# Performance work log

Measured on AMD Instinct MI355X. Metric: run time of the kernel, lower is better.

The kernel has to match this reference:

```python
import jax, jax.numpy as jnp
import numpy as np

NEG_SLOPE = 0.01  # F.leaky_relu default


def gcn_conv(x, W, b, src, dst):
    """PyG GCNConv: add self-loops, symmetric deg^-1/2 normalization, linear, scatter-add."""
    n = x.shape[0]
    loop = jnp.arange(n)
    s = jnp.concatenate([src, loop])  # source j
    d = jnp.concatenate([dst, loop])  # target i
    deg = jax.ops.segment_sum(jnp.ones_like(d, dtype=x.dtype), d, num_segments=n)
    dis = jnp.where(deg > 0, jax.lax.rsqrt(jnp.maximum(deg, 1e-12)), 0.0)
    norm = dis[s] * dis[d]                       # [E+N]
    h = x @ W                                    # [N, out]
    msg = h[s] * norm[:, None]                   # gather + scale
    out = jax.ops.segment_sum(msg, d, num_segments=n)  # scatter-add to targets
    return out + b


def setup_inputs() -> dict:
    key = jax.random.key(0)
    ks = jax.random.split(key, 8)
    N, E, G = 100000, 800000, 100
    IN, H, OUT = 128, 256, 16
    x = jax.random.normal(ks[0], (N, IN), dtype=jnp.float32)
    edge_index = jax.random.randint(ks[1], (2, E), 0, N, dtype=jnp.int64)
    batch = jnp.repeat(jnp.arange(G, dtype=jnp.int64), N // G)  # sorted graph ids
    def glorot(k, fi, fo):
        lim = np.sqrt(6.0 / (fi + fo))
        return jax.random.uniform(k, (fi, fo), jnp.float32, -lim, lim)
    return {
        "x": x, "edge_index": edge_index, "batch": batch,
        "W1": glorot(ks[2], IN, H), "b1": jnp.zeros((H,), jnp.float32),
        "W2": glorot(ks[3], H, H),  "b2": jnp.zeros((H,), jnp.float32),
        "W3": glorot(ks[4], H, OUT), "b3": jnp.zeros((OUT,), jnp.float32),
    }


def reference(x, edge_index, batch, W1, b1, W2, b2, W3, b3):
    src, dst = edge_index[0], edge_index[1]
    h = gcn_conv(x, W1, b1, src, dst)
    h = jax.nn.leaky_relu(h, NEG_SLOPE)  # dropout p=0.0 -> identity
    h = gcn_conv(h, W2, b2, src, dst)
    h = jax.nn.leaky_relu(h, NEG_SLOPE)
    h = gcn_conv(h, W3, b3, src, dst)
    # get_zero_nodes: first node of each graph in the sorted batch vector
    mask = jnp.concatenate([jnp.array([True]), batch[1:] != batch[:-1]])
    return h[mask, :]  # [n_graphs, out_channels]
```

## Files before the change

### kernel.cpp

```cpp
#include <hip/hip_runtime.h>

#define NEG_SLOPE 0.01f

using short8 = __attribute__((ext_vector_type(8))) short;
using f32x4  = __attribute__((ext_vector_type(4))) float;

__device__ inline float b2f(ushort u) {
    union { unsigned u; float f; } x; x.u = ((unsigned)u) << 16; return x.f;
}
__device__ inline ushort f2b(float f) {
    union { float f; unsigned u; } x; x.f = f;
    unsigned r = x.u + 0x7FFFu + ((x.u >> 16) & 1u);
    return (ushort)(r >> 16);
}
__device__ inline void gload16(const void* g, void* l) {
    __builtin_amdgcn_global_load_lds((__attribute__((address_space(1))) void*)g,
                                     (__attribute__((address_space(3))) void*)l, 16, 0, 0);
}


__global__ void init_kernel(const int* __restrict__ batch, int* __restrict__ cnt,
                            int* __restrict__ flag1, int* __restrict__ flag2,
                            int* __restrict__ rootflag, int* __restrict__ picked,
                            int4* __restrict__ aggslot, int N) {
    int i = blockIdx.x * blockDim.x + threadIdx.x;
    if (i < 1024) aggslot[i] = make_int4(0, 0, 0, 0);
    if (i >= N) return;
    cnt[i] = 0;
    int root = (i == 0) || (batch[i] != batch[i - 1]);
    flag1[i] = root;
    flag2[i] = 0;
    rootflag[i] = root;
    if (root) picked[batch[i]] = i;
}


__global__ void count_f1(const int* __restrict__ src, const int* __restrict__ dst,
                         const int* __restrict__ rootflag, int* __restrict__ cnt,
                         int* __restrict__ flag1, int E) {
    int i = blockIdx.x * blockDim.x + threadIdx.x;
    int e0 = i * 4;
    if (e0 + 3 < E) {
        int4 dq = *(const int4*)(dst + e0);
        int r0 = rootflag[dq.x], r1 = rootflag[dq.y], r2 = rootflag[dq.z], r3 = rootflag[dq.w];
        atomicAdd(&cnt[dq.x], 1);
        atomicAdd(&cnt[dq.y], 1);
        atomicAdd(&cnt[dq.z], 1);
        atomicAdd(&cnt[dq.w], 1);
        if (r0 | r1 | r2 | r3) {
            int4 sq = *(const int4*)(src + e0);
            if (r0) flag1[sq.x] = 1;
            if (r1) flag1[sq.y] = 1;
            if (r2) flag1[sq.z] = 1;
            if (r3) flag1[sq.w] = 1;
        }
    } else if (e0 < E) {
        for (int e = e0; e < E; e++) {
            int d = dst[e];
            atomicAdd(&cnt[d], 1);
            if (rootflag[d]) flag1[src[e]] = 1;
        }
    }
}


__global__ void frontier2v(const int* __restrict__ src, const int* __restrict__ dst,
                           const int* __restrict__ flag1, int* __restrict__ flag2,
                           int E, int N) {
    int i = blockIdx.x * blockDim.x + threadIdx.x;
    int e0 = i * 4;
    if (e0 + 3 < E) {
        int4 dq = *(const int4*)(dst + e0);
        int f0 = flag1[dq.x], f1 = flag1[dq.y], f2 = flag1[dq.z], f3 = flag1[dq.w];
        if (f0 | f1 | f2 | f3) {
            int4 sq = *(const int4*)(src + e0);
            if (f0) flag2[sq.x] = 1;
            if (f1) flag2[sq.y] = 1;
            if (f2) flag2[sq.z] = 1;
            if (f3) flag2[sq.w] = 1;
        }
    } else if (e0 < E) {
        for (int e = e0; e < E; e++) if (flag1[dst[e]]) flag2[src[e]] = 1;
    }
    if (i < N && flag1[i]) flag2[i] = 1;
}


__global__ __launch_bounds__(256) void scan_one(
    const int* __restrict__ cnt, const int* __restrict__ f1, const int* __restrict__ f2,
    int4* __restrict__ aggslot, float* __restrict__ dis,
    int* __restrict__ rowptr, int* __restrict__ cur,
    int* __restrict__ pos1, int* __restrict__ pos2,
    int* __restrict__ list1, int* __restrict__ list2,
    int* __restrict__ counts, int N, int nb,
    const float* __restrict__ W1, ushort* __restrict__ W1t,
    const float* __restrict__ W2, ushort* __restrict__ W2t) {
    __shared__ int l0[256], l1[256], l2[256];
    __shared__ int baseS[3];
    const int b = blockIdx.x, t = threadIdx.x;
    const int base = b * 1024 + t * 4;

    int c[4] = {0,0,0,0}, a1[4] = {0,0,0,0}, a2[4] = {0,0,0,0};
    if (base + 3 < N) {
        int4 q = *(const int4*)(cnt + base); c[0]=q.x; c[1]=q.y; c[2]=q.z; c[3]=q.w;
        int4 u = *(const int4*)(f1 + base);  a1[0]=u.x; a1[1]=u.y; a1[2]=u.z; a1[3]=u.w;
        int4 v = *(const int4*)(f2 + base);  a2[0]=v.x; a2[1]=v.y; a2[2]=v.z; a2[3]=v.w;
    } else {
        for (int i = 0; i < 4; i++) if (base + i < N) {
            c[i] = cnt[base + i]; a1[i] = f1[base + i]; a2[i] = f2[base + i];
        }
    }
#pragma unroll
    for (int i = 0; i < 4; i++)
        if (base + i < N) dis[base + i] = rsqrtf((float)c[i] + 1.0f);

    int m[4];
#pragma unroll
    for (int i = 0; i < 4; i++) m[i] = a2[i] ? c[i] : 0;
    int ts0 = m[0] + m[1] + m[2] + m[3];
    int ts1 = a1[0] + a1[1] + a1[2] + a1[3];
    int ts2 = a2[0] + a2[1] + a2[2] + a2[3];
    l0[t] = ts0; l1[t] = ts1; l2[t] = ts2;
    __syncthreads();
    for (int off = 1; off < 256; off <<= 1) {
        int u0 = (t >= off) ? l0[t - off] : 0;
        int u1 = (t >= off) ? l1[t - off] : 0;
        int u2 = (t >= off) ? l2[t - off] : 0;
        __syncthreads();
        l0[t] += u0; l1[t] += u1; l2[t] += u2;
        __syncthreads();
    }

    if (t == 0) {
        __hip_atomic_store(&aggslot[b].x, l0[255], __ATOMIC_RELAXED, __HIP_MEMORY_SCOPE_AGENT);
        __hip_atomic_store(&aggslot[b].y, l1[255], __ATOMIC_RELAXED, __HIP_MEMORY_SCOPE_AGENT);
        __hip_atomic_store(&aggslot[b].z, l2[255], __ATOMIC_RELAXED, __HIP_MEMORY_SCOPE_AGENT);
        __hip_atomic_store(&aggslot[b].w, 1, __ATOMIC_RELEASE, __HIP_MEMORY_SCOPE_AGENT);
    }

    if (t < 64) {
        int g0 = 0, g1 = 0, g2 = 0;
        for (int w0 = 0; w0 < b; w0 += 64) {
            int idx = w0 + t;
            if (idx < b) {
                while (__hip_atomic_load(&aggslot[idx].w, __ATOMIC_ACQUIRE,
                                         __HIP_MEMORY_SCOPE_AGENT) == 0) {
                    __builtin_amdgcn_s_sleep(1);
                }
                g0 += __hip_atomic_load(&aggslot[idx].x, __ATOMIC_RELAXED, __HIP_MEMORY_SCOPE_AGENT);
                g1 += __hip_atomic_load(&aggslot[idx].y, __ATOMIC_RELAXED, __HIP_MEMORY_SCOPE_AGENT);
                g2 += __hip_atomic_load(&aggslot[idx].z, __ATOMIC_RELAXED, __HIP_MEMORY_SCOPE_AGENT);
            }
        }
#pragma unroll
        for (int s = 1; s < 64; s <<= 1) {
            g0 += __shfl_xor(g0, s, 64);
            g1 += __shfl_xor(g1, s, 64);
            g2 += __shfl_xor(g2, s, 64);
        }
        if (t == 0) { baseS[0] = g0; baseS[1] = g1; baseS[2] = g2; }
    }
    __syncthreads();

    int run0 = baseS[0] + l0[t] - ts0;
    int run1 = baseS[1] + l1[t] - ts1;
    int run2 = baseS[2] + l2[t] - ts2;
#pragma unroll
    for (int i = 0; i < 4; i++) {
        if (base + i < N) {
            rowptr[base + i] = run0;
            cur[base + i] = run0;
            if (a1[i]) { pos1[base + i] = run1; list1[run1] = base + i; }
            if (a2[i]) { pos2[base + i] = run2; list2[run2] = base + i; }
        }
        run0 += m[i]; run1 += a1[i]; run2 += a2[i];
    }
    if (b == nb - 1 && t == 255) {
        counts[0] = baseS[1] + l1[255];
        counts[1] = baseS[2] + l2[255];
        rowptr[N] = baseS[0] + l0[255];
    }

    for (int idx = b * 256 + t; idx < 98304; idx += gridDim.x * 256) {
        if (idx < 32768) {
            int n = idx >> 7, k = idx & 127;
            W1t[idx] = f2b(W1[k * 256 + n]);
        } else {
            int j = idx - 32768;
            int n = j >> 8, k = j & 255;
            W2t[j] = f2b(W2[k * 256 + n]);
        }
    }
}


__global__ void fill_fv(const int* __restrict__ src, const int* __restrict__ dst,
                        const int* __restrict__ flag2, int* __restrict__ cur,
                        int* __restrict__ col, int E) {
    int i = blockIdx.x * blockDim.x + threadIdx.x;
    int e0 = i * 4;
    if (e0 + 3 < E) {
        int4 dq = *(const int4*)(dst + e0);
        int f0 = flag2[dq.x], f1 = flag2[dq.y], f2 = flag2[dq.z], f3 = flag2[dq.w];
        if (f0 | f1 | f2 | f3) {
            int4 sq = *(const int4*)(src + e0);
            if (f0) col[atomicAdd(&cur[dq.x], 1)] = sq.x;
            if (f1) col[atomicAdd(&cur[dq.y], 1)] = sq.y;
            if (f2) col[atomicAdd(&cur[dq.z], 1)] = sq.z;
            if (f3) col[atomicAdd(&cur[dq.w], 1)] = sq.w;
        }
    } else if (e0 < E) {
        for (int e = e0; e < E; e++) {
            int d = dst[e];
            if (flag2[d]) col[atomicAdd(&cur[d], 1)] = src[e];
        }
    }
}


__global__ __launch_bounds__(256) void aggx_c(const float* __restrict__ x,
                                              const float* __restrict__ dis,
                                              const int* __restrict__ rowptr,
                                              const int* __restrict__ col,
                                              const int* __restrict__ list2,
                                              const int* __restrict__ counts,
                                              ushort* __restrict__ aggXc) {
    const int M2 = counts[1];
    int wave = blockIdx.x * 4 + (threadIdx.x >> 6);
    int lane = threadIdx.x & 63;
    int li = lane & 31, sub = lane >> 5;
    int stride = gridDim.x * 8;
    const float* xp = x + li * 4;
    for (int p = wave * 2 + sub; p < M2; p += stride) {
        int node = list2[p];
        float di = dis[node];
        float4 sv = *(const float4*)(xp + (size_t)node * 128);
        float a0 = di * sv.x, a1 = di * sv.y, a2 = di * sv.z, a3 = di * sv.w;
        int e = rowptr[node], e1 = rowptr[node + 1];
        for (; e + 2 <= e1; e += 2) {
            int s0 = col[e], s1 = col[e + 1];
            float w0 = dis[s0], w1 = dis[s1];
            float4 v0 = *(const float4*)(xp + (size_t)s0 * 128);
            float4 v1 = *(const float4*)(xp + (size_t)s1 * 128);
            a0 += w0 * v0.x + w1 * v1.x;
            a1 += w0 * v0.y + w1 * v1.y;
            a2 += w0 * v0.z + w1 * v1.z;
            a3 += w0 * v0.w + w1 * v1.w;
        }
        if (e < e1) {
            int s = col[e];
            float w = dis[s];
            float4 v = *(const float4*)(xp + (size_t)s * 128);
            a0 += w * v.x; a1 += w * v.y; a2 += w * v.z; a3 += w * v.w;
        }
        ushort4 o;
        o.x = f2b(di * a0); o.y = f2b(di * a1); o.z = f2b(di * a2); o.w = f2b(di * a3);
        *(ushort4*)(aggXc + (size_t)p * 128 + li * 4) = o;
    }
}


__global__ __launch_bounds__(256) void agg2_c(const ushort* __restrict__ h1c,
                                              const float* __restrict__ dis,
                                              const int* __restrict__ rowptr,
                                              const int* __restrict__ col,
                                              const int* __restrict__ list1,
                                              const int* __restrict__ pos2,
                                              const int* __restrict__ counts,
                                              ushort* __restrict__ agg1c) {
    const int M1 = counts[0];
    int wave = blockIdx.x * 4 + (threadIdx.x >> 6);
    int lane = threadIdx.x & 63;
    int li = lane & 31, sub = lane >> 5;
    int stride = gridDim.x * 8;
    const ushort* hp = h1c + (size_t)li * 8;
    for (int p = wave * 2 + sub; p < M1; p += stride) {
        int i = list1[p];
        float di = dis[i];
        float a[8];
        {
            short8 v = *(const short8*)(hp + (size_t)pos2[i] * 256);
#pragma unroll
            for (int j = 0; j < 8; j++) a[j] = b2f((ushort)v[j]);
        }
        int e1 = rowptr[i + 1];
        for (int e = rowptr[i]; e < e1; e++) {
            short8 v = *(const short8*)(hp + (size_t)pos2[col[e]] * 256);
#pragma unroll
            for (int j = 0; j < 8; j++) a[j] += b2f((ushort)v[j]);
        }
        short8 o;
#pragma unroll
        for (int j = 0; j < 8; j++) o[j] = (short)f2b(di * a[j]);
        *(short8*)(agg1c + (size_t)p * 256 + li * 8) = o;
    }
}


template <int K>
__global__ __launch_bounds__(512) void gemm_c(const ushort* __restrict__ A,
                                              const ushort* __restrict__ Bt,
                                              const float* __restrict__ bias,
                                              const float* __restrict__ dis,
                                              const int* __restrict__ list,
                                              const int* __restrict__ counts, int which,
                                              ushort* __restrict__ C) {
    __shared__ ushort As[128 * 64];
    __shared__ ushort Bs[256 * 64];
    const int M = counts[which];
    const int t = threadIdx.x;
    const int lane = t & 63;
    const int w = t >> 6;
    const int wm = w >> 2, wn = w & 3;

    for (int tile = blockIdx.x; tile * 128 < M; tile += gridDim.x) {
        const int row0 = tile * 128;
        f32x4 acc[4][4] = {};

        for (int kt = 0; kt < K / 64; kt++) {
#pragma unroll
            for (int it = 0; it < 2; it++) {
                int q = it * 512 + t;
                int r = q >> 3, c = q & 7;
                int cs = c ^ (r & 7);
                int ga = min(row0 + r, M - 1);
                gload16(A + (size_t)ga * K + kt * 64 + cs * 8, &As[q * 8]);
            }
#pragma unroll
            for (int it = 0; it < 4; it++) {
                int q = it * 512 + t;
                int r = q >> 3, c = q & 7;
                int cs = c ^ (r & 7);
                gload16(Bt + (size_t)r * K + kt * 64 + cs * 8, &Bs[q * 8]);
            }
            __syncthreads();
#pragma unroll
            for (int ks = 0; ks < 2; ks++) {
                short8 a[4], b[4];
                int cc = ks * 4 + (lane >> 4);
#pragma unroll
                for (int m = 0; m < 4; m++) {
                    int R = wm * 64 + m * 16 + (lane & 15);
                    a[m] = *(const short8*)&As[R * 64 + ((cc ^ (R & 7)) * 8)];
                }
#pragma unroll
                for (int n = 0; n < 4; n++) {
                    int R = wn * 64 + n * 16 + (lane & 15);
                    b[n] = *(const short8*)&Bs[R * 64 + ((cc ^ (R & 7)) * 8)];
                }
#pragma unroll
                for (int m = 0; m < 4; m++)
#pragma unroll
                    for (int n = 0; n < 4; n++)
                        acc[m][n] = __builtin_amdgcn_mfma_f32_16x16x32_bf16(a[m], b[n], acc[m][n], 0, 0, 0);
            }
            __syncthreads();
        }

#pragma unroll
        for (int m = 0; m < 4; m++) {
#pragma unroll
            for (int j = 0; j < 4; j++) {
                int grow = row0 + wm * 64 + m * 16 + (lane >> 4) * 4 + j;
                if (grow >= M) continue;
                float dr = dis[list[grow]];
#pragma unroll
                for (int n = 0; n < 4; n++) {
                    int gcol = wn * 64 + n * 16 + (lane & 15);
                    float v = acc[m][n][j] + bias[gcol];
                    v = v > 0.f ? v : NEG_SLOPE * v;
                    C[(size_t)grow * 256 + gcol] = f2b(v * dr);
                }
            }
        }
    }
}


__global__ __launch_bounds__(256) void final_c(const ushort* __restrict__ h2c,
                                               const float* __restrict__ dis,
                                               const int* __restrict__ rowptr,
                                               const int* __restrict__ col,
                                               const int* __restrict__ picked,
                                               const int* __restrict__ pos1,
                                               const float* __restrict__ W3,
                                               const float* __restrict__ b3,
                                               float* __restrict__ out, int G) {
    __shared__ float agg[256];
    __shared__ float red[256];
    int g = blockIdx.x;
    int t = threadIdx.x;
    if (g >= G) return;
    int i = picked[g];
    float di = dis[i];
    float a = b2f(h2c[(size_t)pos1[i] * 256 + t]);
    int e1 = rowptr[i + 1];
    for (int e = rowptr[i]; e < e1; e++) {
        a += b2f(h2c[(size_t)pos1[col[e]] * 256 + t]);
    }
    agg[t] = di * a;
    __syncthreads();
    int c = t & 15, seg = t >> 4;
    float p = 0.f;
#pragma unroll
    for (int kk = 0; kk < 16; kk++) {
        int k = seg * 16 + kk;
        p += agg[k] * W3[k * 16 + c];
    }
    red[t] = p;
    __syncthreads();
    if (t < 16) {
        float sres = 0.f;
#pragma unroll
        for (int ss = 0; ss < 16; ss++) sres += red[ss * 16 + t];
        out[g * 16 + t] = sres + b3[t];
    }
}


extern "C" void kernel_launch(void* const* d_in, const int* in_sizes, int n_in,
                              void* d_out, int out_size, void* d_ws, size_t ws_size,
                              hipStream_t stream) {
    const float* x   = (const float*)d_in[0];
    const int* ei    = (const int*)d_in[1];
    const int* batch = (const int*)d_in[2];
    const float* W1  = (const float*)d_in[3];
    const float* b1  = (const float*)d_in[4];
    const float* W2  = (const float*)d_in[5];
    const float* b2  = (const float*)d_in[6];
    const float* W3  = (const float*)d_in[7];
    const float* b3  = (const float*)d_in[8];

    const int IN = 128, H = 256, OUT = 16;
    int N = in_sizes[0] / IN;
    int E = in_sizes[1] / 2;
    int G = out_size / OUT;
    const int* srcp = ei;
    const int* dstp = ei + E;

    char* p = (char*)d_ws;
    auto carve = [&](size_t bytes) {
        char* q = p;
        p += (bytes + 255) & ~(size_t)255;
        return q;
    };
    int*    cnt      = (int*)carve((size_t)N * 4);
    int*    flag1    = (int*)carve((size_t)N * 4);
    int*    flag2    = (int*)carve((size_t)N * 4);
    int*    rootflag = (int*)carve((size_t)N * 4);
    float*  dis    = (float*)carve((size_t)N * 4);
    int*    rowptr = (int*)carve(((size_t)N + 1) * 4);
    int*    cur    = (int*)carve((size_t)N * 4);
    int4*   aggslot= (int4*)carve(1024 * 16);
    int*    counts = (int*)carve(256);
    int*    picked = (int*)carve((size_t)G * 4);
    int*    pos1   = (int*)carve((size_t)N * 4);
    int*    pos2   = (int*)carve((size_t)N * 4);
    int*    list1  = (int*)carve((size_t)N * 4);
    int*    list2  = (int*)carve((size_t)N * 4);
    int*    col    = (int*)carve((size_t)E * 4);
    ushort* W1t    = (ushort*)carve((size_t)256 * 128 * 2);
    ushort* W2t    = (ushort*)carve((size_t)256 * 256 * 2);
    ushort* RA     = (ushort*)carve((size_t)N * H * 2);
    ushort* RB     = (ushort*)carve((size_t)N * H * 2);

    ushort* aggXc = RA;
    ushort* agg1c = RA;
    ushort* h1c   = RB;
    ushort* h2c   = RB;

    int nb = (N + 1023) / 1024;
    int e4 = (E + 3) / 4;
    int epN = (e4 > N ? e4 : N);

    init_kernel<<<(N + 255) / 256, 256, 0, stream>>>(batch, cnt, flag1, flag2, rootflag,
                                                     picked, aggslot, N);
    count_f1<<<(e4 + 255) / 256, 256, 0, stream>>>(srcp, dstp, rootflag, cnt, flag1, E);
    frontier2v<<<(epN + 255) / 256, 256, 0, stream>>>(srcp, dstp, flag1, flag2, E, N);
    scan_one<<<nb, 256, 0, stream>>>(cnt, flag1, flag2, aggslot, dis, rowptr, cur,
                                     pos1, pos2, list1, list2, counts, N, nb,
                                     W1, W1t, W2, W2t);
    fill_fv<<<(e4 + 255) / 256, 256, 0, stream>>>(srcp, dstp, flag2, cur, col, E);
    aggx_c<<<1024, 256, 0, stream>>>(x, dis, rowptr, col, list2, counts, aggXc);
    gemm_c<128><<<128, 512, 0, stream>>>(aggXc, W1t, b1, dis, list2, counts, 1, h1c);
    agg2_c<<<128, 256, 0, stream>>>(h1c, dis, rowptr, col, list1, pos2, counts, agg1c);
    gemm_c<256><<<64, 512, 0, stream>>>(agg1c, W2t, b2, dis, list1, counts, 0, h2c);
    final_c<<<G, 256, 0, stream>>>(h2c, dis, rowptr, col, picked, pos1, W3, b3, (float*)d_out, G);
}
```

Measured before the change: 131.3 us.

## Fuse tail GEMM/aggregation stages into persistent kernel with grid barriers

Replaces the four tail launches (GEMM1, second aggregation, GEMM2, final readout) with one persistent 64-block kernel that separates phases with atomic grid barriers. It also drops the init kernel in favour of a memset and computes root flags inline from the batch vector. The aim is to cut launch overhead and inter-kernel gaps on a small problem. In exchange, GEMM1 and the aggregation now run on 64 blocks instead of 128, and the spin barriers assume all blocks are co-resident.

```diff
diff --git a/kernel.cpp b/kernel.cpp
--- a/kernel.cpp
+++ b/kernel.cpp
@@ -17,32 +17,34 @@
     __builtin_amdgcn_global_load_lds((__attribute__((address_space(1))) void*)g,
                                      (__attribute__((address_space(3))) void*)l, 16, 0, 0);
 }
-
-
-__global__ void init_kernel(const int* __restrict__ batch, int* __restrict__ cnt,
-                            int* __restrict__ flag1, int* __restrict__ flag2,
-                            int* __restrict__ rootflag, int* __restrict__ picked,
-                            int4* __restrict__ aggslot, int N) {
+__device__ inline int isroot(const int* __restrict__ batch, int d) {
+    return (d == 0) || (batch[d] != batch[d - 1]);
+}
+__device__ inline void gbar(int* ctr, int nblk) {
+    __syncthreads();
+    if (threadIdx.x == 0) {
+        __threadfence();
+        __hip_atomic_fetch_add(ctr, 1, __ATOMIC_RELEASE, __HIP_MEMORY_SCOPE_AGENT);
+        while (__hip_atomic_load(ctr, __ATOMIC_ACQUIRE, __HIP_MEMORY_SCOPE_AGENT) < nblk)
+            __builtin_amdgcn_s_sleep(1);
+    }
+    __syncthreads();
+}
+
+
+__global__ void count_f1(const int* __restrict__ src, const int* __restrict__ dst,
+                         const int* __restrict__ batch, int* __restrict__ cnt,
+                         int* __restrict__ flag1, int* __restrict__ picked, int E, int N) {
     int i = blockIdx.x * blockDim.x + threadIdx.x;
-    if (i < 1024) aggslot[i] = make_int4(0, 0, 0, 0);
-    if (i >= N) return;
-    cnt[i] = 0;
-    int root = (i == 0) || (batch[i] != batch[i - 1]);
-    flag1[i] = root;
-    flag2[i] = 0;
-    rootflag[i] = root;
-    if (root) picked[batch[i]] = i;
-}
-
-
-__global__ void count_f1(const int* __restrict__ src, const int* __restrict__ dst,
-                         const int* __restrict__ rootflag, int* __restrict__ cnt,
-                         int* __restrict__ flag1, int E) {
-    int i = blockIdx.x * blockDim.x + threadIdx.x;
+    if (i < N && isroot(batch, i)) {
+        picked[batch[i]] = i;
+        flag1[i] = 1;
+    }
     int e0 = i * 4;
     if (e0 + 3 < E) {
         int4 dq = *(const int4*)(dst + e0);
-        int r0 = rootflag[dq.x], r1 = rootflag[dq.y], r2 = rootflag[dq.z], r3 = rootflag[dq.w];
+        int r0 = isroot(batch, dq.x), r1 = isroot(batch, dq.y);
+        int r2 = isroot(batch, dq.z), r3 = isroot(batch, dq.w);
         atomicAdd(&cnt[dq.x], 1);
         atomicAdd(&cnt[dq.y], 1);
         atomicAdd(&cnt[dq.z], 1);
@@ -58,7 +60,7 @@
         for (int e = e0; e < E; e++) {
             int d = dst[e];
             atomicAdd(&cnt[d], 1);
-            if (rootflag[d]) flag1[src[e]] = 1;
+            if (isroot(batch, d)) flag1[src[e]] = 1;
         }
     }
 }
@@ -260,63 +262,20 @@
 }
 
 
-__global__ __launch_bounds__(256) void agg2_c(const ushort* __restrict__ h1c,
-                                              const float* __restrict__ dis,
-                                              const int* __restrict__ rowptr,
-                                              const int* __restrict__ col,
-                                              const int* __restrict__ list1,
-                                              const int* __restrict__ pos2,
-                                              const int* __restrict__ counts,
-                                              ushort* __restrict__ agg1c) {
-    const int M1 = counts[0];
-    int wave = blockIdx.x * 4 + (threadIdx.x >> 6);
-    int lane = threadIdx.x & 63;
-    int li = lane & 31, sub = lane >> 5;
-    int stride = gridDim.x * 8;
-    const ushort* hp = h1c + (size_t)li * 8;
-    for (int p = wave * 2 + sub; p < M1; p += stride) {
-        int i = list1[p];
-        float di = dis[i];
-        float a[8];
-        {
-            short8 v = *(const short8*)(hp + (size_t)pos2[i] * 256);
-#pragma unroll
-            for (int j = 0; j < 8; j++) a[j] = b2f((ushort)v[j]);
-        }
-        int e1 = rowptr[i + 1];
-        for (int e = rowptr[i]; e < e1; e++) {
-            short8 v = *(const short8*)(hp + (size_t)pos2[col[e]] * 256);
-#pragma unroll
-            for (int j = 0; j < 8; j++) a[j] += b2f((ushort)v[j]);
-        }
-        short8 o;
-#pragma unroll
-        for (int j = 0; j < 8; j++) o[j] = (short)f2b(di * a[j]);
-        *(short8*)(agg1c + (size_t)p * 256 + li * 8) = o;
-    }
-}
-
-
 template <int K>
-__global__ __launch_bounds__(512) void gemm_c(const ushort* __restrict__ A,
-                                              const ushort* __restrict__ Bt,
-                                              const float* __restrict__ bias,
-                                              const float* __restrict__ dis,
-                                              const int* __restrict__ list,
-                                              const int* __restrict__ counts, int which,
-                                              ushort* __restrict__ C) {
-    __shared__ ushort As[128 * 64];
-    __shared__ ushort Bs[256 * 64];
-    const int M = counts[which];
+__device__ void gemm_phase(const ushort* __restrict__ A, const ushort* __restrict__ Bt,
+                           const float* __restrict__ bias, const float* __restrict__ dis,
+                           const int* __restrict__ list, int M, ushort* __restrict__ C,
+                           ushort* As, ushort* Bs, int nblk) {
     const int t = threadIdx.x;
     const int lane = t & 63;
     const int w = t >> 6;
     const int wm = w >> 2, wn = w & 3;
 
-    for (int tile = blockIdx.x; tile * 128 < M; tile += gridDim.x) {
+    for (int tile = blockIdx.x; tile * 128 < M; tile += nblk) {
         const int row0 = tile * 128;
         f32x4 acc[4][4] = {};
-
+#pragma unroll
         for (int kt = 0; kt < K / 64; kt++) {
 #pragma unroll
             for (int it = 0; it < 2; it++) {
@@ -356,7 +315,6 @@
             }
             __syncthreads();
         }
-
 #pragma unroll
         for (int m = 0; m < 4; m++) {
 #pragma unroll
@@ -377,43 +335,94 @@
 }
 
 
-__global__ __launch_bounds__(256) void final_c(const ushort* __restrict__ h2c,
-                                               const float* __restrict__ dis,
-                                               const int* __restrict__ rowptr,
-                                               const int* __restrict__ col,
-                                               const int* __restrict__ picked,
-                                               const int* __restrict__ pos1,
-                                               const float* __restrict__ W3,
-                                               const float* __restrict__ b3,
-                                               float* __restrict__ out, int G) {
-    __shared__ float agg[256];
-    __shared__ float red[256];
-    int g = blockIdx.x;
-    int t = threadIdx.x;
-    if (g >= G) return;
-    int i = picked[g];
-    float di = dis[i];
-    float a = b2f(h2c[(size_t)pos1[i] * 256 + t]);
-    int e1 = rowptr[i + 1];
-    for (int e = rowptr[i]; e < e1; e++) {
-        a += b2f(h2c[(size_t)pos1[col[e]] * 256 + t]);
-    }
-    agg[t] = di * a;
-    __syncthreads();
-    int c = t & 15, seg = t >> 4;
-    float p = 0.f;
-#pragma unroll
-    for (int kk = 0; kk < 16; kk++) {
-        int k = seg * 16 + kk;
-        p += agg[k] * W3[k * 16 + c];
-    }
-    red[t] = p;
-    __syncthreads();
-    if (t < 16) {
-        float sres = 0.f;
-#pragma unroll
-        for (int ss = 0; ss < 16; ss++) sres += red[ss * 16 + t];
-        out[g * 16 + t] = sres + b3[t];
+#define TAIL_NBLK 64
+
+__global__ __launch_bounds__(512) void megatail(
+    const ushort* __restrict__ aggXc, const ushort* __restrict__ W1t,
+    const float* __restrict__ b1, ushort* __restrict__ h1c,
+    const float* __restrict__ dis, const int* __restrict__ rowptr,
+    const int* __restrict__ col, const int* __restrict__ list1,
+    const int* __restrict__ list2, const int* __restrict__ pos1,
+    const int* __restrict__ pos2, const int* __restrict__ counts,
+    ushort* __restrict__ agg1c, const ushort* __restrict__ W2t,
+    const float* __restrict__ b2, ushort* __restrict__ h2c,
+    const int* __restrict__ picked, const float* __restrict__ W3,
+    const float* __restrict__ b3, float* __restrict__ out,
+    int* __restrict__ bars, int G) {
+    __shared__ ushort As[128 * 64];
+    __shared__ ushort Bs[256 * 64];
+    __shared__ float aggf[256];
+    __shared__ float redf[256];
+    const int t = threadIdx.x;
+    const int bid = blockIdx.x;
+    const int M1 = counts[0];
+    const int M2 = counts[1];
+
+    gemm_phase<128>(aggXc, W1t, b1, dis, list2, M2, h1c, As, Bs, TAIL_NBLK);
+    gbar(&bars[0], TAIL_NBLK);
+
+    {
+        int lane = t & 63;
+        int w = t >> 6;
+        int wave = bid * 8 + w;
+        int li = lane & 31, sub = lane >> 5;
+        int stride = TAIL_NBLK * 16;
+        const ushort* hp = h1c + (size_t)li * 8;
+        for (int p = wave * 2 + sub; p < M1; p += stride) {
+            int i = list1[p];
+            float di = dis[i];
+            float a[8];
+            {
+                short8 v = *(const short8*)(hp + (size_t)pos2[i] * 256);
+#pragma unroll
+                for (int j = 0; j < 8; j++) a[j] = b2f((ushort)v[j]);
+            }
+            int e1 = rowptr[i + 1];
+            for (int e = rowptr[i]; e < e1; e++) {
+                short8 v = *(const short8*)(hp + (size_t)pos2[col[e]] * 256);
+#pragma unroll
+                for (int j = 0; j < 8; j++) a[j] += b2f((ushort)v[j]);
+            }
+            short8 o;
+#pragma unroll
+            for (int j = 0; j < 8; j++) o[j] = (short)f2b(di * a[j]);
+            *(short8*)(agg1c + (size_t)p * 256 + li * 8) = o;
+        }
+    }
+    gbar(&bars[1], TAIL_NBLK);
+
+    gemm_phase<256>(agg1c, W2t, b2, dis, list1, M1, h2c, As, Bs, TAIL_NBLK);
+    gbar(&bars[2], TAIL_NBLK);
+
+    for (int g = bid; g < G; g += TAIL_NBLK) {
+        if (t < 256) {
+            int i = picked[g];
+            float di = dis[i];
+            float a = b2f(h2c[(size_t)pos1[i] * 256 + t]);
+            int e1 = rowptr[i + 1];
+            for (int e = rowptr[i]; e < e1; e++)
+                a += b2f(h2c[(size_t)pos1[col[e]] * 256 + t]);
+            aggf[t] = di * a;
+        }
+        __syncthreads();
+        if (t < 256) {
+            int c = t & 15, seg = t >> 4;
+            float p = 0.f;
+#pragma unroll
+            for (int kk = 0; kk < 16; kk++) {
+                int k = seg * 16 + kk;
+                p += aggf[k] * W3[k * 16 + c];
+            }
+            redf[t] = p;
+        }
+        __syncthreads();
+        if (t < 16) {
+            float s = 0.f;
+#pragma unroll
+            for (int ss = 0; ss < 16; ss++) s += redf[ss * 16 + t];
+            out[g * 16 + t] = s + b3[t];
+        }
+        __syncthreads();
     }
 }
 
@@ -444,14 +453,15 @@
         p += (bytes + 255) & ~(size_t)255;
         return q;
     };
-    int*    cnt      = (int*)carve((size_t)N * 4);
-    int*    flag1    = (int*)carve((size_t)N * 4);
-    int*    flag2    = (int*)carve((size_t)N * 4);
-    int*    rootflag = (int*)carve((size_t)N * 4);
+    int*    cnt    = (int*)carve((size_t)N * 4);
+    int*    flag1  = (int*)carve((size_t)N * 4);
+    int*    flag2  = (int*)carve((size_t)N * 4);
+    int4*   aggslot= (int4*)carve(1024 * 16);
+    int*    bars   = (int*)carve(256);
+    char*   zend   = p;
     float*  dis    = (float*)carve((size_t)N * 4);
     int*    rowptr = (int*)carve(((size_t)N + 1) * 4);
     int*    cur    = (int*)carve((size_t)N * 4);
-    int4*   aggslot= (int4*)carve(1024 * 16);
     int*    counts = (int*)carve(256);
     int*    picked = (int*)carve((size_t)G * 4);
     int*    pos1   = (int*)carve((size_t)N * 4);
@@ -473,17 +483,16 @@
     int e4 = (E + 3) / 4;
     int epN = (e4 > N ? e4 : N);
 
-    init_kernel<<<(N + 255) / 256, 256, 0, stream>>>(batch, cnt, flag1, flag2, rootflag,
-                                                     picked, aggslot, N);
-    count_f1<<<(e4 + 255) / 256, 256, 0, stream>>>(srcp, dstp, rootflag, cnt, flag1, E);
+    hipMemsetAsync(cnt, 0, (size_t)(zend - (char*)cnt), stream);
+    count_f1<<<(epN + 255) / 256, 256, 0, stream>>>(srcp, dstp, batch, cnt, flag1, picked, E, N);
     frontier2v<<<(epN + 255) / 256, 256, 0, stream>>>(srcp, dstp, flag1, flag2, E, N);
     scan_one<<<nb, 256, 0, stream>>>(cnt, flag1, flag2, aggslot, dis, rowptr, cur,
                                      pos1, pos2, list1, list2, counts, N, nb,
                                      W1, W1t, W2, W2t);
     fill_fv<<<(e4 + 255) / 256, 256, 0, stream>>>(srcp, dstp, flag2, cur, col, E);
     aggx_c<<<1024, 256, 0, stream>>>(x, dis, rowptr, col, list2, counts, aggXc);
-    gemm_c<128><<<128, 512, 0, stream>>>(aggXc, W1t, b1, dis, list2, counts, 1, h1c);
-    agg2_c<<<128, 256, 0, stream>>>(h1c, dis, rowptr, col, list1, pos2, counts, agg1c);
-    gemm_c<256><<<64, 512, 0, stream>>>(agg1c, W2t, b2, dis, list1, counts, 0, h2c);
-    final_c<<<G, 256, 0, stream>>>(h2c, dis, rowptr, col, picked, pos1, W3, b3, (float*)d_out, G);
-}
+    megatail<<<TAIL_NBLK, 512, 0, stream>>>(aggXc, W1t, b1, h1c, dis, rowptr, col,
+                                            list1, list2, pos1, pos2, counts, agg1c,
+                                            W2t, b2, h2c, picked, W3, b3,
+                                            (float*)d_out, bars, G);
+}
```

New measurement: 159.2 us. +21.3%, slower.
